# Optimization experiments

Hardware: AMD Instinct MI355X
Metric: run time of the kernel (lower is better)

## Reference

```python
import jax, jax.numpy as jnp
import numpy as np

B, L, C, A = 32, 50, 80, 3
IMG = 480.0
STRIDES = (8, 16, 32)
OBJ_SCALE, NOOBJ_SCALE, CLS_SCALE, COORD_SCALE = 5.0, 1.0, 1.0, 1.0
IOU_IGNORE = 0.6


def setup_inputs() -> dict:
    key = jax.random.key(0)
    ks = jax.random.split(key, 8)
    anchors = jnp.array([[0.05, 0.07], [0.12, 0.15], [0.25, 0.30]], jnp.float32)
    preds0 = jax.random.normal(ks[0], (B, 60, 60, A * (5 + C)), jnp.float32)
    preds1 = jax.random.normal(ks[1], (B, 30, 30, A * (5 + C)), jnp.float32)
    preds2 = jax.random.normal(ks[2], (B, 15, 15, A * (5 + C)), jnp.float32)
    cls = jax.random.randint(ks[3], (B, L, 1), 0, C).astype(jnp.float32)
    xy = jax.random.uniform(ks[4], (B, L, 2), minval=0.2, maxval=0.8)
    wh = jax.random.uniform(ks[5], (B, L, 2), minval=0.05, maxval=0.3)
    valid = (jax.random.uniform(ks[6], (B, L, 1)) < 0.6).astype(jnp.float32)
    # gt_labels in loss layout: [cx, cy, w, h, class], padded boxes have w=h=0
    gt_labels = jnp.concatenate([xy, wh * valid, cls], -1)
    return {"preds0": preds0, "preds1": preds1, "preds2": preds2,
            "gt_labels": gt_labels, "anchors": anchors}


def get_detector_mask(gt, anchors_l, H, W):
    # gt: [B,L,5] (cx,cy,w,h,class) normalized; anchors_l in grid units
    Bv, Lv, _ = gt.shape
    Av = anchors_l.shape[0]
    scale = jnp.array([W, H, W, H], jnp.float32)
    box = gt[..., :4] * scale                                  # grid units
    valid = box[..., 2] > 0.0                                  # [B,L]
    j = jnp.clip(jnp.floor(box[..., 0]), 0, W - 1).astype(jnp.int32)
    i = jnp.clip(jnp.floor(box[..., 1]), 0, H - 1).astype(jnp.int32)
    wh = box[..., 2:4]                                         # [B,L,2]
    inter = jnp.prod(jnp.minimum(wh[:, :, None, :], anchors_l[None, None]), -1)
    iou = inter / (jnp.prod(wh, -1)[..., None]
                   + jnp.prod(anchors_l, -1)[None, None] - inter + 1e-9)
    k = jnp.argmax(iou, -1)                                    # best anchor [B,L]
    b = jnp.arange(Bv, dtype=jnp.int32)[:, None]
    N = Bv * H * W * Av
    flat = ((b * H + i) * W + j) * Av + k
    flat = jnp.where(valid, flat, N)                           # invalid -> sentinel
    mask = jnp.zeros(N + 1, jnp.float32).at[flat.reshape(-1)].set(1.0)[:N]
    mask = mask.reshape(Bv, H, W, Av, 1)
    anc = anchors_l[k]                                         # [B,L,2]
    safe_wh = jnp.where(valid[..., None], wh, 1.0)
    adj = jnp.concatenate([
        (box[..., 0] - j.astype(jnp.float32))[..., None],
        (box[..., 1] - i.astype(jnp.float32))[..., None],
        jnp.log(safe_wh / anc),
        gt[..., 4:5]], -1)                                     # [B,L,5]
    mtb = jnp.zeros((N + 1, 5), jnp.float32).at[flat.reshape(-1)].set(
        adj.reshape(-1, 5))[:N].reshape(Bv, H, W, Av, 5)
    return mask, mtb


def yolo_head(feats, anchors_l):
    Bv, H, W, _ = feats.shape
    Av = anchors_l.shape[0]
    f = feats.reshape(Bv, H, W, Av, 5 + C)
    gy, gx = jnp.meshgrid(jnp.arange(H, dtype=jnp.float32),
                          jnp.arange(W, dtype=jnp.float32), indexing='ij')
    grid = jnp.stack([gx, gy], -1)[None, :, :, None, :]        # [1,H,W,1,2]
    conv = jnp.array([W, H], jnp.float32)
    box_xy = jax.nn.sigmoid(f[..., :2])
    box_wh = jnp.exp(f[..., 2:4])
    pred_xy = (box_xy + grid) / conv                           # normalized
    pred_wh = box_wh * anchors_l / conv
    return f, box_xy, pred_xy, pred_wh


def level_loss(f, box_xy, pred_xy, pred_wh, gt, mask, mtb):
    # IoU of every predicted box against every GT box -> ignore mask
    pmin = (pred_xy - pred_wh * 0.5)[..., None, :]             # [B,H,W,A,1,2]
    pmax = (pred_xy + pred_wh * 0.5)[..., None, :]
    tmin = (gt[..., :2] - gt[..., 2:4] * 0.5)[:, None, None, None]  # [B,1,1,1,L,2]
    tmax = (gt[..., :2] + gt[..., 2:4] * 0.5)[:, None, None, None]
    wh_i = jnp.clip(jnp.minimum(pmax, tmax) - jnp.maximum(pmin, tmin), 0.0)
    inter = jnp.prod(wh_i, -1)                                 # [B,H,W,A,L]
    parea = jnp.prod(pred_wh, -1)[..., None]
    tarea = jnp.prod(gt[..., 2:4], -1)[:, None, None, None]
    iou = inter / (parea + tarea - inter + 1e-9)
    best = jnp.max(iou, -1, keepdims=True)                     # [B,H,W,A,1]
    obj_det = (best > IOU_IGNORE).astype(f.dtype)
    pred_conf = jax.nn.sigmoid(f[..., 4:5])
    no_obj_loss = NOOBJ_SCALE * (1.0 - obj_det) * (1.0 - mask) * pred_conf ** 2
    obj_loss = OBJ_SCALE * mask * (1.0 - pred_conf) ** 2
    pred_class = jax.nn.softmax(f[..., 5:], -1)
    onehot = jax.nn.one_hot(mtb[..., 4].astype(jnp.int32), C, dtype=f.dtype)
    cls_loss = CLS_SCALE * mask * (onehot - pred_class) ** 2
    pred_boxes = jnp.concatenate([box_xy, f[..., 2:4]], -1)
    coord_loss = COORD_SCALE * mask * (mtb[..., :4] - pred_boxes) ** 2
    return 0.5 * (jnp.sum(no_obj_loss) + jnp.sum(obj_loss)
                  + jnp.sum(cls_loss) + jnp.sum(coord_loss))


def decode(f, pred_xy, pred_wh):
    Bv = f.shape[0]
    bmin = (pred_xy - pred_wh * 0.5) * IMG
    bmax = (pred_xy + pred_wh * 0.5) * IMG
    boxes = jnp.concatenate([bmin, bmax], -1).reshape(Bv, -1, 4)
    scores = (jax.nn.sigmoid(f[..., 4:5])
              * jax.nn.softmax(f[..., 5:], -1)).reshape(Bv, -1, C)
    return boxes, scores


def reference(preds0, preds1, preds2, gt_labels, anchors):
    loss = jnp.float32(0.0)
    boxes_l, scores_l = [], []
    for preds, stride in zip((preds0, preds1, preds2), STRIDES):
        H = W = int(IMG) // stride
        anc = anchors * (IMG / stride)                         # grid units
        mask, mtb = get_detector_mask(gt_labels, anc, H, W)
        f, box_xy, pred_xy, pred_wh = yolo_head(preds, anc)
        loss = loss + level_loss(f, box_xy, pred_xy, pred_wh, gt_labels, mask, mtb)
        bx, sc = decode(f, pred_xy, pred_wh)
        boxes_l.append(bx)
        scores_l.append(sc)
    boxes = jnp.concatenate(boxes_l, axis=1)
    scores = jnp.concatenate(scores_l, axis=1)
    return loss, boxes, scores
```

## Files before the change

### kernel.cpp

```cpp
#include <hip/hip_runtime.h>
#include <math.h>

#define BB 32
#define LL 50
#define CC 80
#define AA 3
#define IMGF 480.0f
#define ROWS_TOTAL 14175
#define BOX_OFF 1L
#define SCORE_OFF (1L + (long)BB * ROWS_TOTAL * 4)

#define CB0 10800
#define CB1 2700
#define CB2 675
#define NCELLS (BB * (CB0 + CB1 + CB2))

#define CH0 169
#define CH1 43
#define CH2 11
#define BLK0 (BB * CH0)
#define BLK1 (BB * CH1)
#define BLK2 (BB * CH2)
#define NBLK (BLK0 + BLK1 + BLK2)

#define WS_MATCH 0
#define WS_CREC  (NCELLS * 4)
#define WS_NVAL  (WS_CREC + BB * LL * 8 * 4)
#define WS_ADJ   (WS_NVAL + 128)
#define WS_PART  (WS_ADJ + 3 * BB * LL * 5 * 4)

__global__ void init_kernel(const float* __restrict__ gt, char* __restrict__ ws)
{
    int idx = blockIdx.x * blockDim.x + threadIdx.x;
    int4* mt = (int4*)(ws + WS_MATCH);
    if (idx < NCELLS / 4) mt[idx] = make_int4(-1, -1, -1, -1);
    if (blockIdx.x == 0 && threadIdx.x < BB) {
        int b = threadIdx.x;
        float* cr = (float*)(ws + WS_CREC) + b * LL * 8;
        int n = 0;
        for (int t = 0; t < LL; ++t) {
            const float* g = gt + (b * LL + t) * 5;
            float x = g[0], y = g[1], w = g[2], h = g[3];
            if (w > 0.0f) {
                float* r = cr + n * 8;
                r[0] = x - 0.5f * w; r[1] = y - 0.5f * h;
                r[2] = x + 0.5f * w; r[3] = y + 0.5f * h;
                r[4] = 0.6f * (w * h); r[5] = 0.f; r[6] = 0.f; r[7] = 0.f;
                n++;
            }
        }
        ((int*)(ws + WS_NVAL))[b] = n;
    }
}

__global__ void prep_kernel(const float* __restrict__ gt,
                            const float* __restrict__ anchors,
                            char* __restrict__ ws)
{
    int idx = blockIdx.x * blockDim.x + threadIdx.x;
    if (idx >= 3 * BB * LL) return;
    int t   = idx % LL;
    int b   = (idx / LL) % BB;
    int lvl = idx / (LL * BB);
    int W       = (lvl == 0) ? 60 : (lvl == 1) ? 30 : 15;
    int cells_b = (lvl == 0) ? CB0 : (lvl == 1) ? CB1 : CB2;
    int cellof  = (lvl == 0) ? 0 : (lvl == 1) ? BB * CB0 : BB * (CB0 + CB1);
    float Wf = (float)W;

    const float* g = gt + (b * LL + t) * 5;
    float x = g[0], y = g[1], wd = g[2], ht = g[3], cls = g[4];
    if (wd <= 0.0f) return;
    float bx = x * Wf, by = y * Wf, bw = wd * Wf, bh = ht * Wf;
    int j = min(max((int)floorf(bx), 0), W - 1);
    int i = min(max((int)floorf(by), 0), W - 1);

    float best = -1.0f; int k = 0; float kaw = 1.0f, kah = 1.0f;
#pragma unroll
    for (int kk = 0; kk < AA; ++kk) {
        float aw = anchors[kk * 2 + 0] * Wf;
        float ah = anchors[kk * 2 + 1] * Wf;
        float inter = fminf(bw, aw) * fminf(bh, ah);
        float iou = inter / (bw * bh + aw * ah - inter + 1e-9f);
        if (iou > best) { best = iou; k = kk; kaw = aw; kah = ah; }
    }
    int cell = (i * W + j) * AA + k;
    atomicMax((int*)(ws + WS_MATCH) + cellof + b * cells_b + cell, t);
    float* ad = (float*)(ws + WS_ADJ) + ((lvl * BB + b) * LL + t) * 5;
    ad[0] = bx - (float)j;
    ad[1] = by - (float)i;
    ad[2] = logf(bw / kaw);
    ad[3] = logf(bh / kah);
    ad[4] = cls;
}

__global__ __launch_bounds__(256) void main_kernel(
    const float* __restrict__ preds0,
    const float* __restrict__ preds1,
    const float* __restrict__ preds2,
    const float* __restrict__ anchors,
    const char* __restrict__ wsc,
    float* __restrict__ partials,
    float* __restrict__ out)
{
    const int*   matchtbl = (const int*)(wsc + WS_MATCH);
    const float* crec     = (const float*)(wsc + WS_CREC);
    const int*   nval     = (const int*)(wsc + WS_NVAL);
    const float* adj      = (const float*)(wsc + WS_ADJ);

    int bid = blockIdx.x;
    const float* preds; int W, cells_b, rowoff, cellof, b, chunk, lvl;
    float invW; unsigned Wmagic;
    if (bid < BLK0) {
        lvl = 0; preds = preds0; W = 60; invW = 1.0f / 60.0f; Wmagic = 71582789u;
        cells_b = CB0; rowoff = 0; cellof = 0;
        b = bid / CH0; chunk = bid - b * CH0;
    } else if (bid < BLK0 + BLK1) {
        int inner = bid - BLK0;
        lvl = 1; preds = preds1; W = 30; invW = 1.0f / 30.0f; Wmagic = 143165577u;
        cells_b = CB1; rowoff = CB0; cellof = BB * CB0;
        b = inner / CH1; chunk = inner - b * CH1;
    } else {
        int inner = bid - BLK0 - BLK1;
        lvl = 2; preds = preds2; W = 15; invW = 1.0f / 15.0f; Wmagic = 286331154u;
        cells_b = CB2; rowoff = CB0 + CB1; cellof = BB * (CB0 + CB1);
        b = inner / CH2; chunk = inner - b * CH2;
    }

    int tid = threadIdx.x;
    int g   = tid >> 2;
    int sub = tid & 3;
    int cell = chunk * 64 + g;
    bool cvalid = cell < cells_b;
    int cc = cvalid ? cell : (cells_b - 1);

    int t1 = cc / 3;
    int a  = cc - t1 * 3;
    int h  = (int)__umulhi((unsigned)t1, Wmagic);
    int w  = t1 - h * W;

    long pbase = ((long)b * cells_b + cc) * 85;
    const float* p = preds + pbase;
    float f0 = p[0], f1 = p[1], f2 = p[2], f3 = p[3], f4 = p[4];

    const float* pc = p + 5 + 4 * sub;
    float4 q0 = *(const float4*)(pc);
    float4 q1 = *(const float4*)(pc + 16);
    float4 q2 = *(const float4*)(pc + 32);
    float4 q3 = *(const float4*)(pc + 48);
    float4 q4 = *(const float4*)(pc + 64);
    q0.x = __expf(q0.x); q0.y = __expf(q0.y); q0.z = __expf(q0.z); q0.w = __expf(q0.w);
    q1.x = __expf(q1.x); q1.y = __expf(q1.y); q1.z = __expf(q1.z); q1.w = __expf(q1.w);
    q2.x = __expf(q2.x); q2.y = __expf(q2.y); q2.z = __expf(q2.z); q2.w = __expf(q2.w);
    q3.x = __expf(q3.x); q3.y = __expf(q3.y); q3.z = __expf(q3.z); q3.w = __expf(q3.w);
    q4.x = __expf(q4.x); q4.y = __expf(q4.y); q4.z = __expf(q4.z); q4.w = __expf(q4.w);
    float s = (q0.x + q0.y + q0.z + q0.w) + (q1.x + q1.y + q1.z + q1.w)
            + (q2.x + q2.y + q2.z + q2.w) + (q3.x + q3.y + q3.z + q3.w)
            + (q4.x + q4.y + q4.z + q4.w);
    s += __shfl_xor(s, 1);
    s += __shfl_xor(s, 2);
    float invs = __builtin_amdgcn_rcpf(s);

    float conf = __builtin_amdgcn_rcpf(1.0f + __expf(-f4));
    float bxs  = __builtin_amdgcn_rcpf(1.0f + __expf(-f0));
    float bys  = __builtin_amdgcn_rcpf(1.0f + __expf(-f1));
    float ancw = anchors[2 * a], anch = anchors[2 * a + 1];
    float pw = __expf(f2) * ancw;
    float ph = __expf(f3) * anch;
    float px = (bxs + (float)w) * invW;
    float py = (bys + (float)h) * invW;
    float pminx = px - 0.5f * pw, pmaxx = px + 0.5f * pw;
    float pminy = py - 0.5f * ph, pmaxy = py + 0.5f * ph;
    float pa06 = 0.6f * (pw * ph) + 0.6e-9f;

    int nv = nval[b];
    const float* cb = crec + b * LL * 8;
    float amax = -1.0f;
    for (int t = sub; t < nv; t += 4) {
        const float* r = cb + t * 8;
        float4 tb = *(const float4*)r;
        float ta06 = r[4];
        float ix = fmaxf(fminf(pmaxx, tb.z) - fmaxf(pminx, tb.x), 0.0f);
        float iy = fmaxf(fminf(pmaxy, tb.w) - fmaxf(pminy, tb.y), 0.0f);
        amax = fmaxf(amax, 1.6f * (ix * iy) - (pa06 + ta06));
    }
    unsigned long long bal = __ballot(amax > 0.0f);
    bool objdet = ((bal >> (tid & 60)) & 0xFULL) != 0ULL;

    int wt = matchtbl[cellof + b * cells_b + cc];

    float partial = 0.0f;
    float ci = conf * invs;
    if (cvalid) {
        long rb = (long)b * ROWS_TOTAL + rowoff + cell;
        float* sb = out + SCORE_OFF + rb * CC + 4 * sub;
        float4 o;
        o.x = q0.x * ci; o.y = q0.y * ci; o.z = q0.z * ci; o.w = q0.w * ci; *(float4*)(sb)      = o;
        o.x = q1.x * ci; o.y = q1.y * ci; o.z = q1.z * ci; o.w = q1.w * ci; *(float4*)(sb + 16) = o;
        o.x = q2.x * ci; o.y = q2.y * ci; o.z = q2.z * ci; o.w = q2.w * ci; *(float4*)(sb + 32) = o;
        o.x = q3.x * ci; o.y = q3.y * ci; o.z = q3.z * ci; o.w = q3.w * ci; *(float4*)(sb + 48) = o;
        o.x = q4.x * ci; o.y = q4.y * ci; o.z = q4.z * ci; o.w = q4.w * ci; *(float4*)(sb + 64) = o;
        {
            float comp = (sub == 0) ? pminx : (sub == 1) ? pminy : (sub == 2) ? pmaxx : pmaxy;
            out[BOX_OFF + rb * 4 + sub] = comp * IMGF;
        }

        if (wt >= 0) {
            const float* ar = adj + ((lvl * BB + b) * LL + wt) * 5;
            int label = (int)ar[4];
            int c = 4 * sub;
            float d;
            d = ((c +  0) == label ? 1.0f : 0.0f) - q0.x * invs; partial += d * d;
            d = ((c +  1) == label ? 1.0f : 0.0f) - q0.y * invs; partial += d * d;
            d = ((c +  2) == label ? 1.0f : 0.0f) - q0.z * invs; partial += d * d;
            d = ((c +  3) == label ? 1.0f : 0.0f) - q0.w * invs; partial += d * d;
            d = ((c + 16) == label ? 1.0f : 0.0f) - q1.x * invs; partial += d * d;
            d = ((c + 17) == label ? 1.0f : 0.0f) - q1.y * invs; partial += d * d;
            d = ((c + 18) == label ? 1.0f : 0.0f) - q1.z * invs; partial += d * d;
            d = ((c + 19) == label ? 1.0f : 0.0f) - q1.w * invs; partial += d * d;
            d = ((c + 32) == label ? 1.0f : 0.0f) - q2.x * invs; partial += d * d;
            d = ((c + 33) == label ? 1.0f : 0.0f) - q2.y * invs; partial += d * d;
            d = ((c + 34) == label ? 1.0f : 0.0f) - q2.z * invs; partial += d * d;
            d = ((c + 35) == label ? 1.0f : 0.0f) - q2.w * invs; partial += d * d;
            d = ((c + 48) == label ? 1.0f : 0.0f) - q3.x * invs; partial += d * d;
            d = ((c + 49) == label ? 1.0f : 0.0f) - q3.y * invs; partial += d * d;
            d = ((c + 50) == label ? 1.0f : 0.0f) - q3.z * invs; partial += d * d;
            d = ((c + 51) == label ? 1.0f : 0.0f) - q3.w * invs; partial += d * d;
            d = ((c + 64) == label ? 1.0f : 0.0f) - q4.x * invs; partial += d * d;
            d = ((c + 65) == label ? 1.0f : 0.0f) - q4.y * invs; partial += d * d;
            d = ((c + 66) == label ? 1.0f : 0.0f) - q4.z * invs; partial += d * d;
            d = ((c + 67) == label ? 1.0f : 0.0f) - q4.w * invs; partial += d * d;
            if (sub == 0) {
                float c0 = ar[0] - bxs, c1 = ar[1] - bys;
                float c2 = ar[2] - f2,  c3 = ar[3] - f3;
                partial += c0 * c0 + c1 * c1 + c2 * c2 + c3 * c3;
                float u = 1.0f - conf;
                partial += 5.0f * u * u;
            }
        } else if (sub == 0) {
            partial += (objdet ? 0.0f : 1.0f) * conf * conf;
        }
    }

    float vsum = partial;
#pragma unroll
    for (int off = 32; off; off >>= 1) vsum += __shfl_xor(vsum, off);
    __shared__ float red[4];
    int wave = tid >> 6;
    if ((tid & 63) == 0) red[wave] = vsum;
    __syncthreads();
    if (tid == 0) partials[bid] = 0.5f * (red[0] + red[1] + red[2] + red[3]);
}

__global__ void reduce_kernel(const float* __restrict__ partials,
                              float* __restrict__ out)
{
    __shared__ float red[4];
    float s = 0.0f;
    for (int i = threadIdx.x; i < NBLK; i += 256) s += partials[i];
#pragma unroll
    for (int off = 32; off; off >>= 1) s += __shfl_xor(s, off);
    int wave = threadIdx.x >> 6;
    if ((threadIdx.x & 63) == 0) red[wave] = s;
    __syncthreads();
    if (threadIdx.x == 0) out[0] = red[0] + red[1] + red[2] + red[3];
}

extern "C" void kernel_launch(void* const* d_in, const int* in_sizes, int n_in,
                              void* d_out, int out_size, void* d_ws, size_t ws_size,
                              hipStream_t stream)
{
    const float* preds0  = (const float*)d_in[0];
    const float* preds1  = (const float*)d_in[1];
    const float* preds2  = (const float*)d_in[2];
    const float* gt      = (const float*)d_in[3];
    const float* anchors = (const float*)d_in[4];
    float* out = (float*)d_out;
    char* ws = (char*)d_ws;

    init_kernel<<<(NCELLS / 4 + 255) / 256, 256, 0, stream>>>(gt, ws);
    prep_kernel<<<(3 * BB * LL + 255) / 256, 256, 0, stream>>>(gt, anchors, ws);
    main_kernel<<<NBLK, 256, 0, stream>>>(preds0, preds1, preds2, anchors,
                                          (const char*)ws,
                                          (float*)(ws + WS_PART), out);
    reduce_kernel<<<1, 256, 0, stream>>>((const float*)(ws + WS_PART), out);
}
```

Before: 320.6 us.

## Stage prediction tile and score output through LDS for coalesced access

The kernel now copies each block's contiguous 64-cell prediction slice (85 floats per cell) into shared memory with float4 loads, then reads its per-thread values from LDS, replacing strided unaligned global loads. Scores are written to an LDS tile and then stored to global memory as one contiguous, 16-byte aligned stream (with a 3-float head offset). The per-image GT records are also cached in LDS for the IoU loop. This adds two extra barriers and about 23 KB of LDS per block, which may lower occupancy.

```diff
diff --git a/kernel.cpp b/kernel.cpp
--- a/kernel.cpp
+++ b/kernel.cpp
@@ -102,6 +102,10 @@
     float* __restrict__ partials,
     float* __restrict__ out)
 {
+    __shared__ __align__(16) float lds[5448];
+    __shared__ __align__(16) float gtrec[LL * 8];
+    __shared__ float red[4];
+
     const int*   matchtbl = (const int*)(wsc + WS_MATCH);
     const float* crec     = (const float*)(wsc + WS_CREC);
     const int*   nval     = (const int*)(wsc + WS_NVAL);
@@ -129,33 +133,42 @@
     int tid = threadIdx.x;
     int g   = tid >> 2;
     int sub = tid & 3;
-    int cell = chunk * 64 + g;
-    bool cvalid = cell < cells_b;
-    int cc = cvalid ? cell : (cells_b - 1);
-
-    int t1 = cc / 3;
-    int a  = cc - t1 * 3;
-    int h  = (int)__umulhi((unsigned)t1, Wmagic);
-    int w  = t1 - h * W;
-
-    long pbase = ((long)b * cells_b + cc) * 85;
-    const float* p = preds + pbase;
-    float f0 = p[0], f1 = p[1], f2 = p[2], f3 = p[3], f4 = p[4];
-
-    const float* pc = p + 5 + 4 * sub;
-    float4 q0 = *(const float4*)(pc);
-    float4 q1 = *(const float4*)(pc + 16);
-    float4 q2 = *(const float4*)(pc + 32);
-    float4 q3 = *(const float4*)(pc + 48);
-    float4 q4 = *(const float4*)(pc + 64);
-    q0.x = __expf(q0.x); q0.y = __expf(q0.y); q0.z = __expf(q0.z); q0.w = __expf(q0.w);
-    q1.x = __expf(q1.x); q1.y = __expf(q1.y); q1.z = __expf(q1.z); q1.w = __expf(q1.w);
-    q2.x = __expf(q2.x); q2.y = __expf(q2.y); q2.z = __expf(q2.z); q2.w = __expf(q2.w);
-    q3.x = __expf(q3.x); q3.y = __expf(q3.y); q3.z = __expf(q3.z); q3.w = __expf(q3.w);
-    q4.x = __expf(q4.x); q4.y = __expf(q4.y); q4.z = __expf(q4.z); q4.w = __expf(q4.w);
-    float s = (q0.x + q0.y + q0.z + q0.w) + (q1.x + q1.y + q1.z + q1.w)
-            + (q2.x + q2.y + q2.z + q2.w) + (q3.x + q3.y + q3.z + q3.w)
-            + (q4.x + q4.y + q4.z + q4.w);
+    int ncell = cells_b - chunk * 64; if (ncell > 64) ncell = 64;
+    bool cvalid = g < ncell;
+    int lc = cvalid ? g : (ncell - 1);
+    int cellg = chunk * 64 + lc;
+
+    long S = ((long)b * cells_b + chunk * 64) * 85;
+    int off0 = (int)(S & 3);
+    long Sa = S - off0;
+    int nf = off0 + ncell * 85;
+    int n4 = nf >> 2;
+    const float4* s4 = (const float4*)(preds + Sa);
+    for (int i = tid; i < n4; i += 256) ((float4*)lds)[i] = s4[i];
+    if (tid < (nf & 3)) lds[(n4 << 2) + tid] = preds[Sa + (n4 << 2) + tid];
+
+    if (tid < 100) ((float4*)gtrec)[tid] = ((const float4*)(crec + b * LL * 8))[tid];
+
+    int wt = matchtbl[cellof + b * cells_b + cellg];
+    int nv = nval[b];
+    __syncthreads();
+
+    int base = off0 + lc * 85;
+    float f0 = lds[base + 0], f1 = lds[base + 1], f2 = lds[base + 2];
+    float f3 = lds[base + 3], f4 = lds[base + 4];
+    float q[20];
+#pragma unroll
+    for (int k = 0; k < 5; ++k)
+#pragma unroll
+        for (int j = 0; j < 4; ++j)
+            q[4 * k + j] = lds[base + 5 + 4 * sub + 16 * k + j];
+    __syncthreads();
+
+#pragma unroll
+    for (int k = 0; k < 20; ++k) q[k] = __expf(q[k]);
+    float s = 0.0f;
+#pragma unroll
+    for (int k = 0; k < 20; ++k) s += q[k];
     s += __shfl_xor(s, 1);
     s += __shfl_xor(s, 2);
     float invs = __builtin_amdgcn_rcpf(s);
@@ -163,72 +176,44 @@
     float conf = __builtin_amdgcn_rcpf(1.0f + __expf(-f4));
     float bxs  = __builtin_amdgcn_rcpf(1.0f + __expf(-f0));
     float bys  = __builtin_amdgcn_rcpf(1.0f + __expf(-f1));
+
+    int t1 = cellg / 3;
+    int a  = cellg - t1 * 3;
+    int hh = (int)__umulhi((unsigned)t1, Wmagic);
+    int ww = t1 - hh * W;
     float ancw = anchors[2 * a], anch = anchors[2 * a + 1];
     float pw = __expf(f2) * ancw;
     float ph = __expf(f3) * anch;
-    float px = (bxs + (float)w) * invW;
-    float py = (bys + (float)h) * invW;
+    float px = (bxs + (float)ww) * invW;
+    float py = (bys + (float)hh) * invW;
     float pminx = px - 0.5f * pw, pmaxx = px + 0.5f * pw;
     float pminy = py - 0.5f * ph, pmaxy = py + 0.5f * ph;
     float pa06 = 0.6f * (pw * ph) + 0.6e-9f;
 
-    int nv = nval[b];
-    const float* cb = crec + b * LL * 8;
     float amax = -1.0f;
     for (int t = sub; t < nv; t += 4) {
-        const float* r = cb + t * 8;
-        float4 tb = *(const float4*)r;
-        float ta06 = r[4];
-        float ix = fmaxf(fminf(pmaxx, tb.z) - fmaxf(pminx, tb.x), 0.0f);
-        float iy = fmaxf(fminf(pmaxy, tb.w) - fmaxf(pminy, tb.y), 0.0f);
-        amax = fmaxf(amax, 1.6f * (ix * iy) - (pa06 + ta06));
+        const float* r = gtrec + t * 8;
+        float ix = fmaxf(fminf(pmaxx, r[2]) - fmaxf(pminx, r[0]), 0.0f);
+        float iy = fmaxf(fminf(pmaxy, r[3]) - fmaxf(pminy, r[1]), 0.0f);
+        amax = fmaxf(amax, 1.6f * (ix * iy) - (pa06 + r[4]));
     }
     unsigned long long bal = __ballot(amax > 0.0f);
     bool objdet = ((bal >> (tid & 60)) & 0xFULL) != 0ULL;
 
-    int wt = matchtbl[cellof + b * cells_b + cc];
-
     float partial = 0.0f;
-    float ci = conf * invs;
     if (cvalid) {
-        long rb = (long)b * ROWS_TOTAL + rowoff + cell;
-        float* sb = out + SCORE_OFF + rb * CC + 4 * sub;
-        float4 o;
-        o.x = q0.x * ci; o.y = q0.y * ci; o.z = q0.z * ci; o.w = q0.w * ci; *(float4*)(sb)      = o;
-        o.x = q1.x * ci; o.y = q1.y * ci; o.z = q1.z * ci; o.w = q1.w * ci; *(float4*)(sb + 16) = o;
-        o.x = q2.x * ci; o.y = q2.y * ci; o.z = q2.z * ci; o.w = q2.w * ci; *(float4*)(sb + 32) = o;
-        o.x = q3.x * ci; o.y = q3.y * ci; o.z = q3.z * ci; o.w = q3.w * ci; *(float4*)(sb + 48) = o;
-        o.x = q4.x * ci; o.y = q4.y * ci; o.z = q4.z * ci; o.w = q4.w * ci; *(float4*)(sb + 64) = o;
-        {
-            float comp = (sub == 0) ? pminx : (sub == 1) ? pminy : (sub == 2) ? pmaxx : pmaxy;
-            out[BOX_OFF + rb * 4 + sub] = comp * IMGF;
-        }
-
         if (wt >= 0) {
             const float* ar = adj + ((lvl * BB + b) * LL + wt) * 5;
             int label = (int)ar[4];
             int c = 4 * sub;
-            float d;
-            d = ((c +  0) == label ? 1.0f : 0.0f) - q0.x * invs; partial += d * d;
-            d = ((c +  1) == label ? 1.0f : 0.0f) - q0.y * invs; partial += d * d;
-            d = ((c +  2) == label ? 1.0f : 0.0f) - q0.z * invs; partial += d * d;
-            d = ((c +  3) == label ? 1.0f : 0.0f) - q0.w * invs; partial += d * d;
-            d = ((c + 16) == label ? 1.0f : 0.0f) - q1.x * invs; partial += d * d;
-            d = ((c + 17) == label ? 1.0f : 0.0f) - q1.y * invs; partial += d * d;
-            d = ((c + 18) == label ? 1.0f : 0.0f) - q1.z * invs; partial += d * d;
-            d = ((c + 19) == label ? 1.0f : 0.0f) - q1.w * invs; partial += d * d;
-            d = ((c + 32) == label ? 1.0f : 0.0f) - q2.x * invs; partial += d * d;
-            d = ((c + 33) == label ? 1.0f : 0.0f) - q2.y * invs; partial += d * d;
-            d = ((c + 34) == label ? 1.0f : 0.0f) - q2.z * invs; partial += d * d;
-            d = ((c + 35) == label ? 1.0f : 0.0f) - q2.w * invs; partial += d * d;
-            d = ((c + 48) == label ? 1.0f : 0.0f) - q3.x * invs; partial += d * d;
-            d = ((c + 49) == label ? 1.0f : 0.0f) - q3.y * invs; partial += d * d;
-            d = ((c + 50) == label ? 1.0f : 0.0f) - q3.z * invs; partial += d * d;
-            d = ((c + 51) == label ? 1.0f : 0.0f) - q3.w * invs; partial += d * d;
-            d = ((c + 64) == label ? 1.0f : 0.0f) - q4.x * invs; partial += d * d;
-            d = ((c + 65) == label ? 1.0f : 0.0f) - q4.y * invs; partial += d * d;
-            d = ((c + 66) == label ? 1.0f : 0.0f) - q4.z * invs; partial += d * d;
-            d = ((c + 67) == label ? 1.0f : 0.0f) - q4.w * invs; partial += d * d;
+#pragma unroll
+            for (int k = 0; k < 5; ++k)
+#pragma unroll
+                for (int j = 0; j < 4; ++j) {
+                    float d = ((c + 16 * k + j) == label ? 1.0f : 0.0f)
+                            - q[4 * k + j] * invs;
+                    partial += d * d;
+                }
             if (sub == 0) {
                 float c0 = ar[0] - bxs, c1 = ar[1] - bys;
                 float c2 = ar[2] - f2,  c3 = ar[3] - f3;
@@ -241,13 +226,40 @@
         }
     }
 
+    float ci = conf * invs;
+    if (cvalid) {
+        float* srow = lds + g * 80 + 4 * sub;
+#pragma unroll
+        for (int k = 0; k < 5; ++k) {
+            float4 o = make_float4(q[4 * k + 0] * ci, q[4 * k + 1] * ci,
+                                   q[4 * k + 2] * ci, q[4 * k + 3] * ci);
+            *(float4*)(srow + 16 * k) = o;
+        }
+        long rb = (long)b * ROWS_TOTAL + rowoff + cellg;
+        float comp = (sub == 0) ? pminx : (sub == 1) ? pminy
+                   : (sub == 2) ? pmaxx : pmaxy;
+        out[BOX_OFF + rb * 4 + sub] = comp * IMGF;
+    }
+
     float vsum = partial;
 #pragma unroll
     for (int off = 32; off; off >>= 1) vsum += __shfl_xor(vsum, off);
-    __shared__ float red[4];
-    int wave = tid >> 6;
-    if ((tid & 63) == 0) red[wave] = vsum;
-    __syncthreads();
+    if ((tid & 63) == 0) red[tid >> 6] = vsum;
+    __syncthreads();
+
+    int rbase = b * ROWS_TOTAL + rowoff + chunk * 64;
+    float* gdst = out + SCORE_OFF + (long)rbase * CC;
+    int nfs = ncell * 80;
+    if (tid < 3) gdst[tid] = lds[tid];
+    int nbody = (nfs - 3) >> 2;
+    float4* d4 = (float4*)(gdst + 3);
+    for (int i = tid; i < nbody; i += 256) {
+        int j = 3 + (i << 2);
+        d4[i] = make_float4(lds[j], lds[j + 1], lds[j + 2], lds[j + 3]);
+    }
+    int tailo = 3 + (nbody << 2);
+    if (tid < (nfs - tailo)) gdst[tailo + tid] = lds[tailo + tid];
+
     if (tid == 0) partials[bid] = 0.5f * (red[0] + red[1] + red[2] + red[3]);
 }
 
```

Measured after the change: 327.8 us. +2.2%, slower.

## Replace per-cell match table with in-kernel matching against compacted GT list

Applied to the files above, without the earlier changes.

Removes the init kernel that filled a match table with one entry per cell, and the prep kernel that scattered matches with atomics. A single small setup kernel now compacts the valid GT boxes per image with a ballot and stores each box's best-anchor index per level. The main kernel recomputes which GT maps to each cell inside its existing IoU loop, then derives the regression targets on the fly. This saves a launch and the table traffic, at the cost of a few extra ALU ops per GT per thread.

```diff
diff --git a/kernel.cpp b/kernel.cpp
--- a/kernel.cpp
+++ b/kernel.cpp
@@ -13,7 +13,6 @@
 #define CB0 10800
 #define CB1 2700
 #define CB2 675
-#define NCELLS (BB * (CB0 + CB1 + CB2))
 
 #define CH0 169
 #define CH1 43
@@ -23,74 +22,47 @@
 #define BLK2 (BB * CH2)
 #define NBLK (BLK0 + BLK1 + BLK2)
 
-#define WS_MATCH 0
-#define WS_CREC  (NCELLS * 4)
-#define WS_NVAL  (WS_CREC + BB * LL * 8 * 4)
-#define WS_ADJ   (WS_NVAL + 128)
-#define WS_PART  (WS_ADJ + 3 * BB * LL * 5 * 4)
-
-__global__ void init_kernel(const float* __restrict__ gt, char* __restrict__ ws)
-{
-    int idx = blockIdx.x * blockDim.x + threadIdx.x;
-    int4* mt = (int4*)(ws + WS_MATCH);
-    if (idx < NCELLS / 4) mt[idx] = make_int4(-1, -1, -1, -1);
-    if (blockIdx.x == 0 && threadIdx.x < BB) {
-        int b = threadIdx.x;
-        float* cr = (float*)(ws + WS_CREC) + b * LL * 8;
-        int n = 0;
-        for (int t = 0; t < LL; ++t) {
-            const float* g = gt + (b * LL + t) * 5;
-            float x = g[0], y = g[1], w = g[2], h = g[3];
-            if (w > 0.0f) {
-                float* r = cr + n * 8;
-                r[0] = x - 0.5f * w; r[1] = y - 0.5f * h;
-                r[2] = x + 0.5f * w; r[3] = y + 0.5f * h;
-                r[4] = 0.6f * (w * h); r[5] = 0.f; r[6] = 0.f; r[7] = 0.f;
-                n++;
+#define WS_CREC  0
+#define WS_NVAL  (BB * LL * 8 * 4)
+#define WS_PART  (WS_NVAL + 128)
+
+__global__ __launch_bounds__(64) void setup_kernel(const float* __restrict__ gt,
+                                                   const float* __restrict__ anchors,
+                                                   char* __restrict__ ws)
+{
+    int b    = blockIdx.x;
+    int lane = threadIdx.x;
+    float x = 0.f, y = 0.f, w = 0.f, h = 0.f, cls = 0.f;
+    bool valid = false;
+    if (lane < LL) {
+        const float* g = gt + (b * LL + lane) * 5;
+        x = g[0]; y = g[1]; w = g[2]; h = g[3]; cls = g[4];
+        valid = (w > 0.0f);
+    }
+    unsigned long long m = __ballot(valid);
+    int pos = (int)__popcll(m & ((1ull << lane) - 1ull));
+    if (lane == 0) ((int*)(ws + WS_NVAL))[b] = (int)__popcll(m);
+    if (valid) {
+        int kpack = 0;
+#pragma unroll
+        for (int lvl = 0; lvl < 3; ++lvl) {
+            float Wf = (lvl == 0) ? 60.f : (lvl == 1) ? 30.f : 15.f;
+            float bw = w * Wf, bh = h * Wf;
+            float best = -1.0f; int kb = 0;
+#pragma unroll
+            for (int kk = 0; kk < AA; ++kk) {
+                float aw = anchors[kk * 2 + 0] * Wf;
+                float ah = anchors[kk * 2 + 1] * Wf;
+                float inter = fminf(bw, aw) * fminf(bh, ah);
+                float iou = inter / (bw * bh + aw * ah - inter + 1e-9f);
+                if (iou > best) { best = iou; kb = kk; }
             }
-        }
-        ((int*)(ws + WS_NVAL))[b] = n;
-    }
-}
-
-__global__ void prep_kernel(const float* __restrict__ gt,
-                            const float* __restrict__ anchors,
-                            char* __restrict__ ws)
-{
-    int idx = blockIdx.x * blockDim.x + threadIdx.x;
-    if (idx >= 3 * BB * LL) return;
-    int t   = idx % LL;
-    int b   = (idx / LL) % BB;
-    int lvl = idx / (LL * BB);
-    int W       = (lvl == 0) ? 60 : (lvl == 1) ? 30 : 15;
-    int cells_b = (lvl == 0) ? CB0 : (lvl == 1) ? CB1 : CB2;
-    int cellof  = (lvl == 0) ? 0 : (lvl == 1) ? BB * CB0 : BB * (CB0 + CB1);
-    float Wf = (float)W;
-
-    const float* g = gt + (b * LL + t) * 5;
-    float x = g[0], y = g[1], wd = g[2], ht = g[3], cls = g[4];
-    if (wd <= 0.0f) return;
-    float bx = x * Wf, by = y * Wf, bw = wd * Wf, bh = ht * Wf;
-    int j = min(max((int)floorf(bx), 0), W - 1);
-    int i = min(max((int)floorf(by), 0), W - 1);
-
-    float best = -1.0f; int k = 0; float kaw = 1.0f, kah = 1.0f;
-#pragma unroll
-    for (int kk = 0; kk < AA; ++kk) {
-        float aw = anchors[kk * 2 + 0] * Wf;
-        float ah = anchors[kk * 2 + 1] * Wf;
-        float inter = fminf(bw, aw) * fminf(bh, ah);
-        float iou = inter / (bw * bh + aw * ah - inter + 1e-9f);
-        if (iou > best) { best = iou; k = kk; kaw = aw; kah = ah; }
-    }
-    int cell = (i * W + j) * AA + k;
-    atomicMax((int*)(ws + WS_MATCH) + cellof + b * cells_b + cell, t);
-    float* ad = (float*)(ws + WS_ADJ) + ((lvl * BB + b) * LL + t) * 5;
-    ad[0] = bx - (float)j;
-    ad[1] = by - (float)i;
-    ad[2] = logf(bw / kaw);
-    ad[3] = logf(bh / kah);
-    ad[4] = cls;
+            kpack |= kb << (2 * lvl);
+        }
+        float* r = (float*)(ws + WS_CREC) + (b * LL + pos) * 8;
+        r[0] = x; r[1] = y; r[2] = w; r[3] = h;
+        r[4] = cls; r[5] = (float)kpack; r[6] = 0.6f * (w * h); r[7] = 0.f;
+    }
 }
 
 __global__ __launch_bounds__(256) void main_kernel(
@@ -102,29 +74,28 @@
     float* __restrict__ partials,
     float* __restrict__ out)
 {
-    const int*   matchtbl = (const int*)(wsc + WS_MATCH);
-    const float* crec     = (const float*)(wsc + WS_CREC);
-    const int*   nval     = (const int*)(wsc + WS_NVAL);
-    const float* adj      = (const float*)(wsc + WS_ADJ);
+    const float* crec = (const float*)(wsc + WS_CREC);
+    const int*   nval = (const int*)(wsc + WS_NVAL);
 
     int bid = blockIdx.x;
-    const float* preds; int W, cells_b, rowoff, cellof, b, chunk, lvl;
+    const float* preds; int W, cells_b, rowoff, b, chunk, lvl;
     float invW; unsigned Wmagic;
     if (bid < BLK0) {
         lvl = 0; preds = preds0; W = 60; invW = 1.0f / 60.0f; Wmagic = 71582789u;
-        cells_b = CB0; rowoff = 0; cellof = 0;
+        cells_b = CB0; rowoff = 0;
         b = bid / CH0; chunk = bid - b * CH0;
     } else if (bid < BLK0 + BLK1) {
         int inner = bid - BLK0;
         lvl = 1; preds = preds1; W = 30; invW = 1.0f / 30.0f; Wmagic = 143165577u;
-        cells_b = CB1; rowoff = CB0; cellof = BB * CB0;
+        cells_b = CB1; rowoff = CB0;
         b = inner / CH1; chunk = inner - b * CH1;
     } else {
         int inner = bid - BLK0 - BLK1;
         lvl = 2; preds = preds2; W = 15; invW = 1.0f / 15.0f; Wmagic = 286331154u;
-        cells_b = CB2; rowoff = CB0 + CB1; cellof = BB * (CB0 + CB1);
+        cells_b = CB2; rowoff = CB0 + CB1;
         b = inner / CH2; chunk = inner - b * CH2;
     }
+    float Wf = (float)W;
 
     int tid = threadIdx.x;
     int g   = tid >> 2;
@@ -148,6 +119,9 @@
     float4 q2 = *(const float4*)(pc + 32);
     float4 q3 = *(const float4*)(pc + 48);
     float4 q4 = *(const float4*)(pc + 64);
+
+    int nv = nval[b];
+
     q0.x = __expf(q0.x); q0.y = __expf(q0.y); q0.z = __expf(q0.z); q0.w = __expf(q0.w);
     q1.x = __expf(q1.x); q1.y = __expf(q1.y); q1.z = __expf(q1.z); q1.w = __expf(q1.w);
     q2.x = __expf(q2.x); q2.y = __expf(q2.y); q2.z = __expf(q2.z); q2.w = __expf(q2.w);
@@ -172,21 +146,52 @@
     float pminy = py - 0.5f * ph, pmaxy = py + 0.5f * ph;
     float pa06 = 0.6f * (pw * ph) + 0.6e-9f;
 
-    int nv = nval[b];
     const float* cb = crec + b * LL * 8;
     float amax = -1.0f;
+    int wtloc = -1;
     for (int t = sub; t < nv; t += 4) {
         const float* r = cb + t * 8;
-        float4 tb = *(const float4*)r;
-        float ta06 = r[4];
-        float ix = fmaxf(fminf(pmaxx, tb.z) - fmaxf(pminx, tb.x), 0.0f);
-        float iy = fmaxf(fminf(pmaxy, tb.w) - fmaxf(pminy, tb.y), 0.0f);
-        amax = fmaxf(amax, 1.6f * (ix * iy) - (pa06 + ta06));
+        float4 rA = *(const float4*)r;
+        float4 rB = *(const float4*)(r + 4);
+        float tminx = rA.x - 0.5f * rA.z, tmaxx = rA.x + 0.5f * rA.z;
+        float tminy = rA.y - 0.5f * rA.w, tmaxy = rA.y + 0.5f * rA.w;
+        float ix = fmaxf(fminf(pmaxx, tmaxx) - fmaxf(pminx, tminx), 0.0f);
+        float iy = fmaxf(fminf(pmaxy, tmaxy) - fmaxf(pminy, tminy), 0.0f);
+        amax = fmaxf(amax, 1.6f * (ix * iy) - (pa06 + rB.z));
+        float bxg = rA.x * Wf, byg = rA.y * Wf;
+        int jg = min(max((int)floorf(bxg), 0), W - 1);
+        int ig = min(max((int)floorf(byg), 0), W - 1);
+        int kg = (((int)rB.y) >> (2 * lvl)) & 3;
+        int cellt = (ig * W + jg) * 3 + kg;
+        if (cellt == cc) wtloc = (t > wtloc) ? t : wtloc;
     }
     unsigned long long bal = __ballot(amax > 0.0f);
     bool objdet = ((bal >> (tid & 60)) & 0xFULL) != 0ULL;
 
-    int wt = matchtbl[cellof + b * cells_b + cc];
+    {
+        int o1 = __shfl_xor(wtloc, 1); wtloc = (o1 > wtloc) ? o1 : wtloc;
+        int o2 = __shfl_xor(wtloc, 2); wtloc = (o2 > wtloc) ? o2 : wtloc;
+    }
+    int wt = wtloc;
+
+    float ar0 = 0.f, ar1 = 0.f, ar2 = 0.f, ar3 = 0.f; int label = -1;
+    if (wt >= 0) {
+        const float* r = cb + wt * 8;
+        label = (int)r[4];
+        if (sub == 0) {
+            float bxg = r[0] * Wf, byg = r[1] * Wf;
+            float bwg = r[2] * Wf, bhg = r[3] * Wf;
+            int jg = min(max((int)floorf(bxg), 0), W - 1);
+            int ig = min(max((int)floorf(byg), 0), W - 1);
+            int kg = (((int)r[5]) >> (2 * lvl)) & 3;
+            float kaw = anchors[2 * kg + 0] * Wf;
+            float kah = anchors[2 * kg + 1] * Wf;
+            ar0 = bxg - (float)jg;
+            ar1 = byg - (float)ig;
+            ar2 = logf(bwg / kaw);
+            ar3 = logf(bhg / kah);
+        }
+    }
 
     float partial = 0.0f;
     float ci = conf * invs;
@@ -200,13 +205,12 @@
         o.x = q3.x * ci; o.y = q3.y * ci; o.z = q3.z * ci; o.w = q3.w * ci; *(float4*)(sb + 48) = o;
         o.x = q4.x * ci; o.y = q4.y * ci; o.z = q4.z * ci; o.w = q4.w * ci; *(float4*)(sb + 64) = o;
         {
-            float comp = (sub == 0) ? pminx : (sub == 1) ? pminy : (sub == 2) ? pmaxx : pmaxy;
+            float comp = (sub == 0) ? pminx : (sub == 1) ? pminy
+                       : (sub == 2) ? pmaxx : pmaxy;
             out[BOX_OFF + rb * 4 + sub] = comp * IMGF;
         }
 
         if (wt >= 0) {
-            const float* ar = adj + ((lvl * BB + b) * LL + wt) * 5;
-            int label = (int)ar[4];
             int c = 4 * sub;
             float d;
             d = ((c +  0) == label ? 1.0f : 0.0f) - q0.x * invs; partial += d * d;
@@ -230,8 +234,8 @@
             d = ((c + 66) == label ? 1.0f : 0.0f) - q4.z * invs; partial += d * d;
             d = ((c + 67) == label ? 1.0f : 0.0f) - q4.w * invs; partial += d * d;
             if (sub == 0) {
-                float c0 = ar[0] - bxs, c1 = ar[1] - bys;
-                float c2 = ar[2] - f2,  c3 = ar[3] - f3;
+                float c0 = ar0 - bxs, c1 = ar1 - bys;
+                float c2 = ar2 - f2,  c3 = ar3 - f3;
                 partial += c0 * c0 + c1 * c1 + c2 * c2 + c3 * c3;
                 float u = 1.0f - conf;
                 partial += 5.0f * u * u;
@@ -277,8 +281,7 @@
     float* out = (float*)d_out;
     char* ws = (char*)d_ws;
 
-    init_kernel<<<(NCELLS / 4 + 255) / 256, 256, 0, stream>>>(gt, ws);
-    prep_kernel<<<(3 * BB * LL + 255) / 256, 256, 0, stream>>>(gt, anchors, ws);
+    setup_kernel<<<BB, 64, 0, stream>>>(gt, anchors, ws);
     main_kernel<<<NBLK, 256, 0, stream>>>(preds0, preds1, preds2, anchors,
                                           (const char*)ws,
                                           (float*)(ws + WS_PART), out);
```

After: 285.8 us. 10.9% less time.
